# Performance work log

Measured on AMD Instinct MI355X. Metric: run time of the kernel, lower is better.

The kernel has to match this reference:

```python
import jax, jax.numpy as jnp
import numpy as np
import math

D_MODEL = 1024
N_HEADS = 16
D_HEAD = D_MODEL // N_HEADS
DECAY_MAX = 0.99  # buggy torch init: only the LAST head's decay rate survives the loop
LN_EPS = 1e-5


def setup_inputs() -> dict:
    key = jax.random.key(0)
    ks = jax.random.split(key, 12)
    B, S = 2, 2048
    x = jax.random.normal(ks[0], (B, S, D_MODEL), dtype=jnp.float32)
    def w(k):
        return jax.random.normal(k, (D_MODEL, D_MODEL), dtype=jnp.float32) * 0.02
    return {
        "x": x,
        "Wq": w(ks[1]), "bq": jnp.zeros((D_MODEL,), jnp.float32),
        "Wk": w(ks[2]), "bk": jnp.zeros((D_MODEL,), jnp.float32),
        "Wv": w(ks[3]), "bv": jnp.zeros((D_MODEL,), jnp.float32),
        "Wg": w(ks[4]), "bg": jnp.zeros((D_MODEL,), jnp.float32),
        "Wo": w(ks[5]), "bo": jnp.zeros((D_MODEL,), jnp.float32),
        "gamma": jnp.ones((D_MODEL,), jnp.float32),
        "beta": jnp.zeros((D_MODEL,), jnp.float32),
    }


def _decay_mask(S):
    # faithful to torch buffer: decay_matrix[i,j] = DECAY_MAX**(i-j) for j<=i else 0
    i = jnp.arange(S, dtype=jnp.float32)[:, None]
    j = jnp.arange(S, dtype=jnp.float32)[None, :]
    diff = i - j
    return jnp.where(diff >= 0, jnp.power(jnp.float32(DECAY_MAX), diff), 0.0)  # [S,S]


def reference(x, Wq, bq, Wk, bk, Wv, bv, Wg, bg, Wo, bo, gamma, beta):
    B, S, D = x.shape
    H, DH = N_HEADS, D_HEAD
    # projections -> [B,H,S,DH]
    Q = (x @ Wq + bq).reshape(B, S, H, DH).transpose(0, 2, 1, 3)
    K = (x @ Wk + bk).reshape(B, S, H, DH).transpose(0, 2, 1, 3)
    V = (x @ Wv + bv).reshape(B, S, H, DH).transpose(0, 2, 1, 3)
    scores = jnp.einsum('bhsd,bhtd->bhst', Q, K) / math.sqrt(DH)  # [B,H,S,S]
    mask = _decay_mask(S)  # [S,S], broadcast over B,H (head-independent per torch bug)
    retained = jnp.einsum('bhst,bhtd->bhsd', scores * mask, V)
    retained = retained.transpose(0, 2, 1, 3).reshape(B, S, D)
    # LayerNorm over last dim
    mu = jnp.mean(retained, axis=-1, keepdims=True)
    var = jnp.var(retained, axis=-1, keepdims=True)
    normed = (retained - mu) * jax.lax.rsqrt(var + LN_EPS) * gamma + beta
    G = jax.nn.sigmoid(x @ Wg + bg)
    return (normed * G) @ Wo + bo  # dropout = identity (eval)
```

## Files before the change

kernel.cpp:

```cpp
#include <hip/hip_runtime.h>

typedef __attribute__((ext_vector_type(4))) float f32x4;
typedef __attribute__((ext_vector_type(8))) short bf16x8;
typedef unsigned short USHORT;

static __device__ __forceinline__ float bf2f(USHORT u) {
    return __uint_as_float(((unsigned)u) << 16);
}
static __device__ __forceinline__ USHORT f2bf(float f) {
    unsigned u = __float_as_uint(f);
    unsigned r = u + 0x7FFF + ((u >> 16) & 1);
    return (USHORT)(r >> 16);
}

#define GLDS16(gp, lp) __builtin_amdgcn_global_load_lds(                      \
    (const __attribute__((address_space(1))) unsigned int*)(gp),              \
    (__attribute__((address_space(3))) unsigned int*)(lp), 16, 0, 0)

#define FULL_BARRIER() asm volatile("s_waitcnt vmcnt(0) lgkmcnt(0)\ns_barrier" ::: "memory")

#define D64 0.52559648f
#define L2D (-0.014499569695115089f)

struct PrepArgs { const float* src[5]; USHORT* dst[5]; const float* x; USHORT* xb; };

__global__ __launch_bounds__(256) void k_prep(PrepArgs pa) {
    const int z = blockIdx.z;
    const int tid = threadIdx.x;
    __shared__ USHORT t[64][65];
    if (z < 5) {
        const float* __restrict__ W  = pa.src[z];
        USHORT* __restrict__      WT = pa.dst[z];
        const int k0 = blockIdx.y * 64, n0 = blockIdx.x * 64;
#pragma unroll
        for (int s = 0; s < 4; s++) {
            int slot = tid + s * 256;
            int row = slot >> 4, c4 = (slot & 15) * 4;
            float4 vv = *(const float4*)&W[(size_t)(k0 + row) * 1024 + n0 + c4];
            t[row][c4 + 0] = f2bf(vv.x);
            t[row][c4 + 1] = f2bf(vv.y);
            t[row][c4 + 2] = f2bf(vv.z);
            t[row][c4 + 3] = f2bf(vv.w);
        }
        __syncthreads();
#pragma unroll
        for (int s = 0; s < 2; s++) {
            int slot = tid + s * 256;
            int n = slot >> 3, c8 = (slot & 7) * 8;
            USHORT tmp[8];
#pragma unroll
            for (int u = 0; u < 8; u++) tmp[u] = t[c8 + u][n];
            *(int4*)&WT[(size_t)(n0 + n) * 1024 + k0 + c8] = *(int4*)tmp;
        }
    } else {
        const int bi = blockIdx.y * 16 + blockIdx.x;
        const float* xs = pa.x + (size_t)bi * 16384;
        USHORT* xd = pa.xb + (size_t)bi * 16384;
#pragma unroll
        for (int u = 0; u < 16; u++) {
            int idx = u * 1024 + tid * 4;
            float4 v = *(const float4*)&xs[idx];
            *(ushort4*)&xd[idx] = make_ushort4(f2bf(v.x), f2bf(v.y), f2bf(v.z), f2bf(v.w));
        }
    }
}

struct GArgs {
    const USHORT* A;
    const USHORT* W[4];
    const float*  bias[4];
    void*         dst[4];
    USHORT*       dstv;
    float         scale[4];
    int           mode[4];
};


__global__ __launch_bounds__(256, 2) void k_gemm(GArgs ga) {
    const int z = blockIdx.z;
    const USHORT* __restrict__ A  = ga.A;
    const USHORT* __restrict__ BT = ga.W[z];
    __shared__ USHORT As[2][128 * 32];
    __shared__ USHORT Bs[2][128 * 32];
    const int tid = threadIdx.x;
    const int m0 = blockIdx.y * 128, n0 = blockIdx.x * 128;
    const int w = tid >> 6, l = tid & 63, lr = l & 15, q = l >> 4;
    const int wr = w >> 1, wc = w & 1;
    const int srow = tid >> 2, sco = (tid & 3) * 8;
    const int scol = (((tid & 3) ^ ((tid >> 3) & 3)) << 3);
    const int kread = ((q ^ ((lr >> 1) & 3)) << 3);
    f32x4 acc[4][4] = {};
    GLDS16(&A [(size_t)(m0 + srow)      * 1024 + scol], &As[0][srow * 32 + sco]);
    GLDS16(&A [(size_t)(m0 + srow + 64) * 1024 + scol], &As[0][(srow + 64) * 32 + sco]);
    GLDS16(&BT[(size_t)(n0 + srow)      * 1024 + scol], &Bs[0][srow * 32 + sco]);
    GLDS16(&BT[(size_t)(n0 + srow + 64) * 1024 + scol], &Bs[0][(srow + 64) * 32 + sco]);
    for (int kt = 0; kt < 32; kt++) {
        const int cur = kt & 1;
        FULL_BARRIER();
        if (kt + 1 < 32) {
            const int k1 = (kt + 1) * 32;
            const int nxt = 1 - cur;
            GLDS16(&A [(size_t)(m0 + srow)      * 1024 + k1 + scol], &As[nxt][srow * 32 + sco]);
            GLDS16(&A [(size_t)(m0 + srow + 64) * 1024 + k1 + scol], &As[nxt][(srow + 64) * 32 + sco]);
            GLDS16(&BT[(size_t)(n0 + srow)      * 1024 + k1 + scol], &Bs[nxt][srow * 32 + sco]);
            GLDS16(&BT[(size_t)(n0 + srow + 64) * 1024 + k1 + scol], &Bs[nxt][(srow + 64) * 32 + sco]);
        }
        bf16x8 af[4], bfr[4];
#pragma unroll
        for (int mi = 0; mi < 4; mi++)
            af[mi] = *(const bf16x8*)&As[cur][(wr * 64 + mi * 16 + lr) * 32 + kread];
#pragma unroll
        for (int ni = 0; ni < 4; ni++)
            bfr[ni] = *(const bf16x8*)&Bs[cur][(wc * 64 + ni * 16 + lr) * 32 + kread];
#pragma unroll
        for (int mi = 0; mi < 4; mi++)
#pragma unroll
            for (int ni = 0; ni < 4; ni++)
                acc[mi][ni] = __builtin_amdgcn_mfma_f32_16x16x32_bf16(
                    af[mi], bfr[ni], acc[mi][ni], 0, 0, 0);
    }
    const float scale = ga.scale[z];
    const int mode = ga.mode[z];
    const float* __restrict__ bias = ga.bias[z];
#pragma unroll
    for (int ni = 0; ni < 4; ni++) {
        int col = n0 + wc * 64 + ni * 16 + lr;
        float bv = bias[col];
#pragma unroll
        for (int mi = 0; mi < 4; mi++) {
            int r0 = m0 + wr * 64 + mi * 16 + q * 4;
            float vr[4];
#pragma unroll
            for (int r = 0; r < 4; r++) {
                float v = acc[mi][ni][r] + bv;
                if (mode == 1) v = 1.0f / (1.0f + __expf(-v));
                vr[r] = v * scale;
            }
            if (mode == 3) {
                float* df = (float*)ga.dst[z];
#pragma unroll
                for (int r = 0; r < 4; r++)
                    df[(size_t)(r0 + r) * 1024 + col] = vr[r];
            } else if (mode == 2) {
                int b = r0 >> 11, s = r0 & 2047;
                int h = col >> 6, d = col & 63;
                const float NP1 = 1.0101010101010102f;
                float c0 = exp2f(-L2D * (float)(s & 63));
                float c1 = c0 * NP1, c2 = c1 * NP1, c3 = c2 * NP1;
                *(ushort4*)&ga.dstv[(size_t)(((b * 16 + h) * 64) + d) * 2048 + s] =
                    make_ushort4(f2bf(vr[0] * c0), f2bf(vr[1] * c1),
                                 f2bf(vr[2] * c2), f2bf(vr[3] * c3));
            } else {
                USHORT* db = (USHORT*)ga.dst[z];
#pragma unroll
                for (int r = 0; r < 4; r++)
                    db[(size_t)(r0 + r) * 1024 + col] = f2bf(vr[r]);
            }
        }
    }
}

#define LDSA(buf, kh) (((buf) * 2 + (kh)) * 8192)
#define LDSB(buf, kh) (32768 + ((buf) * 2 + (kh)) * 8192)
#define BAR() asm volatile("s_barrier" ::: "memory")
#define VM8() asm volatile("s_waitcnt vmcnt(8)" ::: "memory")

#define STAGE_A(ks, kh, buf) do {                                             \
    const USHORT* s_ = aBase + (ks) * 64 + (kh) * 32;                         \
    GLDS16(s_,          &lds[LDSA(buf, kh) + ldsT]);                          \
    GLDS16(s_ + 131072, &lds[LDSA(buf, kh) + 4096 + ldsT]); } while (0)

#define STAGE_B(ks, kh, buf) do {                                             \
    const USHORT* s_ = bBase + (ks) * 64 + (kh) * 32;                         \
    GLDS16(s_,          &lds[LDSB(buf, kh) + ldsT]);                          \
    GLDS16(s_ + 131072, &lds[LDSB(buf, kh) + 4096 + ldsT]); } while (0)

#define PHASE256(buf, kh, mg, LOADB, STAGE_STMT, WAITSTMT) do {               \
    _Pragma("unroll")                                                         \
    for (int mi = 0; mi < 4; mi++)                                            \
        af[mi] = *(const bf16x8*)&lds[LDSA(buf, kh) + aoff + ((mg) * 4 + mi) * 512]; \
    if (LOADB) {                                                              \
        _Pragma("unroll")                                                     \
        for (int ni = 0; ni < 4; ni++)                                        \
            bfrag[ni] = *(const bf16x8*)&lds[LDSB(buf, kh) + boff + ni * 512];\
    }                                                                         \
    STAGE_STMT;                                                               \
    BAR();                                                                    \
    __builtin_amdgcn_s_setprio(1);                                            \
    _Pragma("unroll")                                                         \
    for (int mi = 0; mi < 4; mi++)                                            \
        _Pragma("unroll")                                                     \
        for (int ni = 0; ni < 4; ni++)                                        \
            acc[(mg) * 4 + mi][ni] = __builtin_amdgcn_mfma_f32_16x16x32_bf16( \
                af[mi], bfrag[ni], acc[(mg) * 4 + mi][ni], 0, 0, 0);          \
    __builtin_amdgcn_s_setprio(0);                                            \
    WAITSTMT;                                                                 \
    BAR();                                                                    \
} while (0)

__global__ __launch_bounds__(512, 2) void k_gemm256(GArgs ga) {
    extern __shared__ USHORT lds[];
    int bid = blockIdx.x + 4 * (blockIdx.y + 16 * blockIdx.z);
    bid = (bid & 7) * 32 + (bid >> 3);
    const int bz = bid >> 6;
    const int by = (bid >> 2) & 15;
    const int bx = bid & 3;
    const int z = bz;
    const USHORT* __restrict__ A  = ga.A;
    const USHORT* __restrict__ BT = ga.W[z];
    const int m0 = by * 256, n0 = bx * 256;
    const int tid = threadIdx.x;
    const int wid = tid >> 6, l = tid & 63, lr = l & 15, q = l >> 4;
    const int wr = wid >> 2, wc = wid & 3;
    const int srow = tid >> 2;
    const int scol = (((tid & 3) ^ ((tid >> 3) & 3)) << 3);
    const USHORT* aBase = A  + (size_t)(m0 + srow) * 1024 + scol;
    const USHORT* bBase = BT + (size_t)(n0 + srow) * 1024 + scol;
    const int ldsT = tid * 8;
    const int kread = ((q ^ ((lr >> 1) & 3)) << 3);
    const int aoff = (wr * 128 + lr) * 32 + kread;
    const int boff = (wc * 64 + lr) * 32 + kread;
    f32x4 acc[8][4] = {};
    bf16x8 af[4], bfrag[4];

    STAGE_A(0, 0, 0); STAGE_B(0, 0, 0);
    STAGE_A(0, 1, 0); STAGE_B(0, 1, 0);
    STAGE_A(1, 0, 1); STAGE_B(1, 0, 1);
    VM8();
    BAR();

    for (int kt = 0; kt < 16; kt += 2) {
        const int ks1 = kt + 1;
        const int ks2 = (kt + 2 < 16) ? kt + 2 : 15;
        const int ks3 = (kt + 2 < 16) ? kt + 2 : 15;
        const int ks4 = (kt + 3 < 16) ? kt + 3 : 15;
        PHASE256(0, 0, 0, 1, STAGE_A(ks1, 1, 1), (void)0);
        PHASE256(0, 0, 1, 0, STAGE_B(ks1, 1, 1), VM8());
        PHASE256(0, 1, 0, 1, STAGE_A(ks2, 0, 0), (void)0);
        PHASE256(0, 1, 1, 0, STAGE_B(ks2, 0, 0), VM8());
        PHASE256(1, 0, 0, 1, STAGE_A(ks3, 1, 0), (void)0);
        PHASE256(1, 0, 1, 0, STAGE_B(ks3, 1, 0), VM8());
        PHASE256(1, 1, 0, 1, STAGE_A(ks4, 0, 1), (void)0);
        PHASE256(1, 1, 1, 0, STAGE_B(ks4, 0, 1), VM8());
    }

    const float scale = ga.scale[z];
    const int mode = ga.mode[z];
    const float* __restrict__ bias = ga.bias[z];
#pragma unroll
    for (int ni = 0; ni < 4; ni++) {
        int col = n0 + wc * 64 + ni * 16 + lr;
        float bv = bias[col];
#pragma unroll
        for (int mi = 0; mi < 8; mi++) {
            int r0 = m0 + wr * 128 + mi * 16 + q * 4;
            float vr[4];
#pragma unroll
            for (int r = 0; r < 4; r++) {
                float v = acc[mi][ni][r] + bv;
                if (mode == 1) v = 1.0f / (1.0f + __expf(-v));
                vr[r] = v * scale;
            }
            if (mode == 3) {
                float* df = (float*)ga.dst[z];
#pragma unroll
                for (int r = 0; r < 4; r++)
                    df[(size_t)(r0 + r) * 1024 + col] = vr[r];
            } else if (mode == 2) {
                int b = r0 >> 11, s = r0 & 2047;
                int h = col >> 6, d = col & 63;
                const float NP1 = 1.0101010101010102f;
                float c0 = exp2f(-L2D * (float)(s & 63));
                float c1 = c0 * NP1, c2 = c1 * NP1, c3 = c2 * NP1;
                *(ushort4*)&ga.dstv[(size_t)(((b * 16 + h) * 64) + d) * 2048 + s] =
                    make_ushort4(f2bf(vr[0] * c0), f2bf(vr[1] * c1),
                                 f2bf(vr[2] * c2), f2bf(vr[3] * c3));
            } else {
                USHORT* db = (USHORT*)ga.dst[z];
#pragma unroll
                for (int r = 0; r < 4; r++)
                    db[(size_t)(r0 + r) * 1024 + col] = f2bf(vr[r]);
            }
        }
    }
}

__global__ __launch_bounds__(256) void k_attn_u(const USHORT* __restrict__ K,
                                                const USHORT* __restrict__ VT,
                                                float* __restrict__ U) {
    const int bh = blockIdx.x, c = blockIdx.y;
    const int b = bh >> 4, h = bh & 15;
    const int tid = threadIdx.x, w = tid >> 6, l = tid & 63, lr = l & 15, q = l >> 4;
    __shared__ USHORT KT[64 * 72];
    __shared__ USHORT Vs[64 * 72];
#pragma unroll
    for (int s = 0; s < 2; s++) {
        int slot = tid + s * 256;
        int row = slot >> 3, co = (slot & 7) * 8;
        USHORT kv[8];
        *(int4*)kv = *(const int4*)&K[(size_t)(b * 2048 + c * 64 + row) * 1024 + h * 64 + co];
#pragma unroll
        for (int u = 0; u < 8; u++) KT[(co + u) * 72 + row] = kv[u];
        *(int4*)&Vs[row * 72 + co] =
            *(const int4*)&VT[(size_t)(bh * 64 + row) * 2048 + c * 64 + co];
    }
    __syncthreads();
    f32x4 acc[4] = {};
    bf16x8 av[2];
#pragma unroll
    for (int kk = 0; kk < 2; kk++)
        av[kk] = *(const bf16x8*)&Vs[(w * 16 + lr) * 72 + kk * 32 + q * 8];
#pragma unroll
    for (int dkt = 0; dkt < 4; dkt++)
#pragma unroll
        for (int kk = 0; kk < 2; kk++) {
            bf16x8 bk = *(const bf16x8*)&KT[(dkt * 16 + lr) * 72 + kk * 32 + q * 8];
            acc[dkt] = __builtin_amdgcn_mfma_f32_16x16x32_bf16(av[kk], bk, acc[dkt], 0, 0, 0);
        }
    float* slot = U + (size_t)(bh * 32 + c) * 4096;
#pragma unroll
    for (int dkt = 0; dkt < 4; dkt++)
#pragma unroll
        for (int r = 0; r < 4; r++)
            slot[(w * 16 + q * 4 + r) * 64 + dkt * 16 + lr] = acc[dkt][r] * D64;
}

__global__ __launch_bounds__(256) void k_scan(float* __restrict__ U) {
    const int bh = blockIdx.x;
    const int idx4 = blockIdx.y * 256 + threadIdx.x;
    float* base = U + (size_t)bh * 32 * 4096 + idx4 * 4;
    float4 s = make_float4(0.f, 0.f, 0.f, 0.f);
    for (int c = 0; c < 32; c++) {
        float* p = base + (size_t)c * 4096;
        float4 v = *(const float4*)p;
        s.x = s.x * D64 + v.x;
        s.y = s.y * D64 + v.y;
        s.z = s.z * D64 + v.z;
        s.w = s.w * D64 + v.w;
        *(float4*)p = s;
    }
}

__global__ __launch_bounds__(256, 2) void k_apply(const USHORT* __restrict__ Q,
                                                  const USHORT* __restrict__ K,
                                                  const USHORT* __restrict__ VT,
                                                  const float* __restrict__ U,
                                                  USHORT* __restrict__ R,
                                                  float* __restrict__ stats) {
    const int bh = blockIdx.x, c = blockIdx.y;
    const int b = bh >> 4, h = bh & 15;
    const int i0 = c * 64;
    const int tid = threadIdx.x, w = tid >> 6, l = tid & 63, lr = l & 15, q = l >> 4;
    __shared__ USHORT Qs[64 * 72];
    __shared__ USHORT Ks[64 * 72];
    __shared__ USHORT Vs[64 * 72];
    __shared__ USHORT Ps[4][16 * 72];
    __shared__ unsigned Spk[4096];
#pragma unroll
    for (int s = 0; s < 2; s++) {
        int slot = tid + s * 256;
        int row = slot >> 3, c8 = (slot & 7) * 8;
        USHORT q8[8];
        *(int4*)q8 = *(const int4*)&Q[(size_t)(b * 2048 + i0 + row) * 1024 + h * 64 + c8];
        const float fr = exp2f(L2D * (float)row);
#pragma unroll
        for (int u = 0; u < 8; u++) q8[u] = f2bf(bf2f(q8[u]) * fr);
        *(int4*)&Qs[row * 72 + c8] = *(int4*)q8;
        *(int4*)&Ks[row * 72 + c8] =
            *(const int4*)&K[(size_t)(b * 2048 + i0 + row) * 1024 + h * 64 + c8];
        *(int4*)&Vs[row * 72 + c8] =
            *(const int4*)&VT[(size_t)(bh * 64 + row) * 2048 + i0 + c8];
    }
    if (c > 0) {
        const float* p = U + (size_t)(bh * 32 + (c - 1)) * 4096 + tid * 16;
        float sa[16];
#pragma unroll
        for (int u4 = 0; u4 < 4; u4++) {
            float4 uv = *(const float4*)(p + u4 * 4);
            sa[u4 * 4 + 0] = uv.x; sa[u4 * 4 + 1] = uv.y;
            sa[u4 * 4 + 2] = uv.z; sa[u4 * 4 + 3] = uv.w;
        }
#pragma unroll
        for (int u = 0; u < 16; u++) {
            USHORT hi = f2bf(sa[u]);
            float  lo = sa[u] - bf2f(hi);
            Spk[tid * 16 + u] = (unsigned)hi | ((unsigned)f2bf(lo) << 16);
        }
    }
    __syncthreads();
    bf16x8 bqf[2];
#pragma unroll
    for (int kk = 0; kk < 2; kk++)
        bqf[kk] = *(const bf16x8*)&Qs[(w * 16 + lr) * 72 + kk * 32 + q * 8];
    f32x4 accr[4] = {};
    if (c > 0) {
#pragma unroll
        for (int dt = 0; dt < 4; dt++)
#pragma unroll
            for (int kk = 0; kk < 2; kk++) {
                const unsigned* sp = &Spk[(dt * 16 + lr) * 64 + kk * 32 + q * 8];
                uint4 pa = *(const uint4*)sp;
                uint4 pb = *(const uint4*)(sp + 4);
                unsigned pk[8] = { pa.x, pa.y, pa.z, pa.w, pb.x, pb.y, pb.z, pb.w };
                bf16x8 hi, lo;
#pragma unroll
                for (int u = 0; u < 8; u++) {
                    hi[u] = (short)(pk[u] & 0xffffu);
                    lo[u] = (short)(pk[u] >> 16);
                }
                accr[dt] = __builtin_amdgcn_mfma_f32_16x16x32_bf16(hi, bqf[kk], accr[dt], 0, 0, 0);
                accr[dt] = __builtin_amdgcn_mfma_f32_16x16x32_bf16(lo, bqf[kk], accr[dt], 0, 0, 0);
            }
    }
    {
        f32x4 accp[4] = {};
#pragma unroll
        for (int kk = 0; kk < 2; kk++)
#pragma unroll
            for (int jt = 0; jt < 4; jt++) {
                bf16x8 akf = *(const bf16x8*)&Ks[(jt * 16 + lr) * 72 + kk * 32 + q * 8];
                accp[jt] = __builtin_amdgcn_mfma_f32_16x16x32_bf16(akf, bqf[kk], accp[jt], 0, 0, 0);
            }
        const int ii = w * 16 + lr;
#pragma unroll
        for (int jt = 0; jt < 4; jt++) {
            const int jj = jt * 16 + q * 4;
            float v0 = (jj + 0 <= ii) ? accp[jt][0] : 0.0f;
            float v1 = (jj + 1 <= ii) ? accp[jt][1] : 0.0f;
            float v2 = (jj + 2 <= ii) ? accp[jt][2] : 0.0f;
            float v3 = (jj + 3 <= ii) ? accp[jt][3] : 0.0f;
            unsigned w0 = __builtin_amdgcn_perm(
                __float_as_uint(v1), __float_as_uint(v0), 0x07060302u);
            unsigned w1 = __builtin_amdgcn_perm(
                __float_as_uint(v3), __float_as_uint(v2), 0x07060302u);
            *(uint2*)&Ps[w][lr * 72 + jt * 16 + q * 4] = make_uint2(w0, w1);
        }
        asm volatile("s_waitcnt lgkmcnt(0)" ::: "memory");
#pragma unroll
        for (int kk = 0; kk < 2; kk++) {
            bf16x8 bpf = *(const bf16x8*)&Ps[w][lr * 72 + kk * 32 + q * 8];
#pragma unroll
            for (int dt = 0; dt < 4; dt++) {
                bf16x8 avf = *(const bf16x8*)&Vs[(dt * 16 + lr) * 72 + kk * 32 + q * 8];
                accr[dt] = __builtin_amdgcn_mfma_f32_16x16x32_bf16(avf, bpf, accr[dt], 0, 0, 0);
            }
        }
    }
    {
        float s1 = 0.f, s2 = 0.f;
#pragma unroll
        for (int dt = 0; dt < 4; dt++)
#pragma unroll
            for (int r = 0; r < 4; r++) {
                float v = accr[dt][r];
                s1 += v; s2 += v * v;
            }
        s1 += __shfl_down(s1, 32); s2 += __shfl_down(s2, 32);
        s1 += __shfl_down(s1, 16); s2 += __shfl_down(s2, 16);
        if (q == 0) {
            int row = b * 2048 + i0 + w * 16 + lr;
            *(float2*)&stats[((size_t)row * 16 + h) * 2] = make_float2(s1, s2);
        }
    }
    {
        const int i = i0 + w * 16 + lr;
#pragma unroll
        for (int dt = 0; dt < 4; dt++) {
            f32x4 a = accr[dt];
            *(ushort4*)&R[(size_t)(b * 2048 + i) * 1024 + h * 64 + dt * 16 + q * 4] =
                make_ushort4(f2bf(a[0]), f2bf(a[1]), f2bf(a[2]), f2bf(a[3]));
        }
    }
}

__global__ __launch_bounds__(256) void k_ln_gate(const USHORT* __restrict__ R,
                                                 const USHORT* __restrict__ G,
                                                 const float* __restrict__ stats,
                                                 const float* __restrict__ gamma,
                                                 const float* __restrict__ beta,
                                                 USHORT* __restrict__ NG) {
    const int row = blockIdx.x, tid = threadIdx.x;
    float s1 = 0.f, s2 = 0.f;
    const float* sp = &stats[(size_t)row * 32];
#pragma unroll
    for (int hh = 0; hh < 8; hh++) {
        float4 v = *(const float4*)(sp + hh * 4);
        s1 += v.x + v.z; s2 += v.y + v.w;
    }
    const float mu  = s1 * (1.0f / 1024.0f);
    const float var = s2 * (1.0f / 1024.0f) - mu * mu;
    const float inv = rsqrtf(fmaxf(var, 0.0f) + 1e-5f);
    ushort4 rv = *(const ushort4*)&R[(size_t)row * 1024 + tid * 4];
    ushort4 g4 = *(const ushort4*)&G[(size_t)row * 1024 + tid * 4];
    float4 gm = *(const float4*)&gamma[tid * 4];
    float4 bt = *(const float4*)&beta[tid * 4];
    float  vv[4]  = { bf2f(rv.x), bf2f(rv.y), bf2f(rv.z), bf2f(rv.w) };
    USHORT gg[4]  = { g4.x, g4.y, g4.z, g4.w };
    float  gmm[4] = { gm.x, gm.y, gm.z, gm.w };
    float  btt[4] = { bt.x, bt.y, bt.z, bt.w };
    USHORT o4[4];
#pragma unroll
    for (int u = 0; u < 4; u++) {
        float nv = (vv[u] - mu) * inv * gmm[u] + btt[u];
        o4[u] = f2bf(nv * bf2f(gg[u]));
    }
    *(ushort4*)&NG[(size_t)row * 1024 + tid * 4] = make_ushort4(o4[0], o4[1], o4[2], o4[3]);
}

extern "C" void kernel_launch(void* const* d_in, const int* in_sizes, int n_in,
                              void* d_out, int out_size, void* d_ws, size_t ws_size,
                              hipStream_t stream) {
    const float* x     = (const float*)d_in[0];
    const float* Wq    = (const float*)d_in[1];
    const float* bq    = (const float*)d_in[2];
    const float* Wk    = (const float*)d_in[3];
    const float* bk    = (const float*)d_in[4];
    const float* Wv    = (const float*)d_in[5];
    const float* bv    = (const float*)d_in[6];
    const float* Wg    = (const float*)d_in[7];
    const float* bg    = (const float*)d_in[8];
    const float* Wo    = (const float*)d_in[9];
    const float* bo    = (const float*)d_in[10];
    const float* gamma = (const float*)d_in[11];
    const float* beta  = (const float*)d_in[12];

    char* ws = (char*)d_ws;
    const size_t MB = 1 << 20;
    USHORT* WqT = (USHORT*)(ws + 0 * MB);
    USHORT* WkT = (USHORT*)(ws + 2 * MB);
    USHORT* WvT = (USHORT*)(ws + 4 * MB);
    USHORT* WgT = (USHORT*)(ws + 6 * MB);
    USHORT* WoT = (USHORT*)(ws + 8 * MB);
    USHORT* Qb  = (USHORT*)(ws + 10 * MB);
    USHORT* Kb  = (USHORT*)(ws + 18 * MB);
    USHORT* VTb = (USHORT*)(ws + 26 * MB);
    USHORT* Gb  = (USHORT*)(ws + 34 * MB);
    float*  Sts = (float*) (ws + 42 * MB);
    USHORT* NGb = Qb;
    USHORT* Xb  = (USHORT*)d_out;
    float*  Ust = (float*)d_out;

    {
        PrepArgs pa;
        pa.src[0] = Wq; pa.src[1] = Wk; pa.src[2] = Wv; pa.src[3] = Wg; pa.src[4] = Wo;
        pa.dst[0] = WqT; pa.dst[1] = WkT; pa.dst[2] = WvT; pa.dst[3] = WgT; pa.dst[4] = WoT;
        pa.x = x; pa.xb = Xb;
        k_prep<<<dim3(16, 16, 6), 256, 0, stream>>>(pa);
    }
    {
        static int s_256ok = -1;
        if (s_256ok < 0) {
            hipError_t e = hipFuncSetAttribute(
                reinterpret_cast<const void*>(&k_gemm256),
                hipFuncAttributeMaxDynamicSharedMemorySize, 131072);
            s_256ok = (e == hipSuccess) ? 1 : 0;
        }
        GArgs ga;
        ga.A = Xb;
        ga.W[0] = WqT; ga.W[1] = WkT; ga.W[2] = WvT; ga.W[3] = WgT;
        ga.bias[0] = bq; ga.bias[1] = bk; ga.bias[2] = bv; ga.bias[3] = bg;
        ga.dst[0] = Qb; ga.dst[1] = Kb; ga.dst[2] = nullptr; ga.dst[3] = Gb;
        ga.dstv = VTb;
        ga.scale[0] = 0.125f; ga.scale[1] = 1.0f; ga.scale[2] = 1.0f; ga.scale[3] = 1.0f;
        ga.mode[0] = 0; ga.mode[1] = 0; ga.mode[2] = 2; ga.mode[3] = 1;
        if (s_256ok)
            k_gemm256<<<dim3(4, 16, 4), 512, 131072, stream>>>(ga);
        else
            k_gemm<<<dim3(8, 32, 4), 256, 0, stream>>>(ga);
    }
    k_attn_u<<<dim3(32, 32), 256, 0, stream>>>(Kb, VTb, Ust);
    k_scan<<<dim3(32, 4), 256, 0, stream>>>(Ust);
    k_apply<<<dim3(32, 32), 256, 0, stream>>>(Qb, Kb, VTb, Ust, Kb, Sts);
    k_ln_gate<<<4096, 256, 0, stream>>>(Kb, Gb, Sts, gamma, beta, NGb);
    {
        GArgs go;
        go.A = NGb;
        for (int i = 0; i < 4; i++) {
            go.W[i] = WoT; go.bias[i] = bo; go.dst[i] = d_out;
            go.scale[i] = 1.0f; go.mode[i] = 3;
        }
        go.dstv = nullptr;
        k_gemm<<<dim3(8, 32, 1), 256, 0, stream>>>(go);
    }
}
```

Baseline: 214.4 us.

## Fold Q decay into GEMM epilogue, pack scan state, use direct-to-LDS swizzled loads

The per-row decay factor on Q moves out of k_apply into the projection GEMM epilogue through a new mode 4. k_scan now writes its state as packed bf16 hi/lo pairs, so k_apply no longer converts it. k_attn_u and k_apply load tiles straight into LDS with global_load_lds using XOR-swizzled unpadded layouts, in place of register staging with padded rows. This cuts VALU conversion work and register round-trips in the attention kernels. The cost is extra epilogue math in the GEMM and a state buffer whose meaning is now reinterpreted between kernels.

```diff
diff --git a/kernel.cpp b/kernel.cpp
--- a/kernel.cpp
+++ b/kernel.cpp
@@ -74,7 +74,6 @@
     float         scale[4];
     int           mode[4];
 };
-
 
 __global__ __launch_bounds__(256, 2) void k_gemm(GArgs ga) {
     const int z = blockIdx.z;
@@ -130,11 +129,14 @@
         for (int mi = 0; mi < 4; mi++) {
             int r0 = m0 + wr * 64 + mi * 16 + q * 4;
             float vr[4];
+            float d0 = (mode == 4) ? exp2f(L2D * (float)(r0 & 63)) : 1.0f;
 #pragma unroll
             for (int r = 0; r < 4; r++) {
                 float v = acc[mi][ni][r] + bv;
                 if (mode == 1) v = 1.0f / (1.0f + __expf(-v));
-                vr[r] = v * scale;
+                v *= scale;
+                if (mode == 4) { v *= d0; d0 *= 0.99f; }
+                vr[r] = v;
             }
             if (mode == 3) {
                 float* df = (float*)ga.dst[z];
@@ -255,11 +257,14 @@
         for (int mi = 0; mi < 8; mi++) {
             int r0 = m0 + wr * 128 + mi * 16 + q * 4;
             float vr[4];
+            float d0 = (mode == 4) ? exp2f(L2D * (float)(r0 & 63)) : 1.0f;
 #pragma unroll
             for (int r = 0; r < 4; r++) {
                 float v = acc[mi][ni][r] + bv;
                 if (mode == 1) v = 1.0f / (1.0f + __expf(-v));
-                vr[r] = v * scale;
+                v *= scale;
+                if (mode == 4) { v *= d0; d0 *= 0.99f; }
+                vr[r] = v;
             }
             if (mode == 3) {
                 float* df = (float*)ga.dst[z];
@@ -292,7 +297,7 @@
     const int b = bh >> 4, h = bh & 15;
     const int tid = threadIdx.x, w = tid >> 6, l = tid & 63, lr = l & 15, q = l >> 4;
     __shared__ USHORT KT[64 * 72];
-    __shared__ USHORT Vs[64 * 72];
+    __shared__ USHORT Vs[64 * 64];
 #pragma unroll
     for (int s = 0; s < 2; s++) {
         int slot = tid + s * 256;
@@ -300,23 +305,32 @@
         USHORT kv[8];
         *(int4*)kv = *(const int4*)&K[(size_t)(b * 2048 + c * 64 + row) * 1024 + h * 64 + co];
 #pragma unroll
-        for (int u = 0; u < 8; u++) KT[(co + u) * 72 + row] = kv[u];
-        *(int4*)&Vs[row * 72 + co] =
-            *(const int4*)&VT[(size_t)(bh * 64 + row) * 2048 + c * 64 + co];
-    }
-    __syncthreads();
+        for (int u = 0; u < 8; u++) {
+            int d = co + u;
+            KT[d * 72 + ((((row >> 3) ^ ((d >> 3) & 7)) << 3) | (row & 7))] = kv[u];
+        }
+        int r_ = slot >> 3, j_ = slot & 7;
+        int js_ = ((j_ ^ (r_ & 7)) << 3);
+        GLDS16(&VT[(size_t)(bh * 64 + r_) * 2048 + c * 64 + js_], &Vs[slot * 8]);
+    }
+    FULL_BARRIER();
     f32x4 acc[4] = {};
     bf16x8 av[2];
-#pragma unroll
-    for (int kk = 0; kk < 2; kk++)
-        av[kk] = *(const bf16x8*)&Vs[(w * 16 + lr) * 72 + kk * 32 + q * 8];
-#pragma unroll
-    for (int dkt = 0; dkt < 4; dkt++)
+    {
+        const int row = w * 16 + lr;
+#pragma unroll
+        for (int kk = 0; kk < 2; kk++)
+            av[kk] = *(const bf16x8*)&Vs[row * 64 + (((kk * 4 + q) ^ (row & 7)) << 3)];
+    }
+#pragma unroll
+    for (int dkt = 0; dkt < 4; dkt++) {
+        const int dp = dkt * 16 + lr;
 #pragma unroll
         for (int kk = 0; kk < 2; kk++) {
-            bf16x8 bk = *(const bf16x8*)&KT[(dkt * 16 + lr) * 72 + kk * 32 + q * 8];
+            bf16x8 bk = *(const bf16x8*)&KT[dp * 72 + (((kk * 4 + q) ^ ((dp >> 3) & 7)) << 3)];
             acc[dkt] = __builtin_amdgcn_mfma_f32_16x16x32_bf16(av[kk], bk, acc[dkt], 0, 0, 0);
         }
+    }
     float* slot = U + (size_t)(bh * 32 + c) * 4096;
 #pragma unroll
     for (int dkt = 0; dkt < 4; dkt++)
@@ -337,68 +351,69 @@
         s.y = s.y * D64 + v.y;
         s.z = s.z * D64 + v.z;
         s.w = s.w * D64 + v.w;
-        *(float4*)p = s;
+        unsigned pk[4];
+        const float sv[4] = { s.x, s.y, s.z, s.w };
+#pragma unroll
+        for (int u = 0; u < 4; u++) {
+            USHORT hi = f2bf(sv[u]);
+            float  lo = sv[u] - bf2f(hi);
+            pk[u] = (unsigned)hi | ((unsigned)f2bf(lo) << 16);
+        }
+        *(uint4*)p = make_uint4(pk[0], pk[1], pk[2], pk[3]);
     }
 }
 
 __global__ __launch_bounds__(256, 2) void k_apply(const USHORT* __restrict__ Q,
                                                   const USHORT* __restrict__ K,
                                                   const USHORT* __restrict__ VT,
-                                                  const float* __restrict__ U,
+                                                  const unsigned* __restrict__ Sp,
                                                   USHORT* __restrict__ R,
                                                   float* __restrict__ stats) {
     const int bh = blockIdx.x, c = blockIdx.y;
     const int b = bh >> 4, h = bh & 15;
     const int i0 = c * 64;
     const int tid = threadIdx.x, w = tid >> 6, l = tid & 63, lr = l & 15, q = l >> 4;
-    __shared__ USHORT Qs[64 * 72];
-    __shared__ USHORT Ks[64 * 72];
-    __shared__ USHORT Vs[64 * 72];
+    __shared__ USHORT Qs[64 * 64];
+    __shared__ USHORT Ks[64 * 64];
+    __shared__ USHORT Vs[64 * 64];
     __shared__ USHORT Ps[4][16 * 72];
     __shared__ unsigned Spk[4096];
 #pragma unroll
     for (int s = 0; s < 2; s++) {
-        int slot = tid + s * 256;
-        int row = slot >> 3, c8 = (slot & 7) * 8;
-        USHORT q8[8];
-        *(int4*)q8 = *(const int4*)&Q[(size_t)(b * 2048 + i0 + row) * 1024 + h * 64 + c8];
-        const float fr = exp2f(L2D * (float)row);
-#pragma unroll
-        for (int u = 0; u < 8; u++) q8[u] = f2bf(bf2f(q8[u]) * fr);
-        *(int4*)&Qs[row * 72 + c8] = *(int4*)q8;
-        *(int4*)&Ks[row * 72 + c8] =
-            *(const int4*)&K[(size_t)(b * 2048 + i0 + row) * 1024 + h * 64 + c8];
-        *(int4*)&Vs[row * 72 + c8] =
-            *(const int4*)&VT[(size_t)(bh * 64 + row) * 2048 + i0 + c8];
+        int C = tid + s * 256;
+        int r_ = C >> 3, j_ = C & 7;
+        int js_ = ((j_ ^ (r_ & 7)) << 3);
+        GLDS16(&Q [(size_t)(b * 2048 + i0 + r_) * 1024 + h * 64 + js_], &Qs[C * 8]);
+        GLDS16(&K [(size_t)(b * 2048 + i0 + r_) * 1024 + h * 64 + js_], &Ks[C * 8]);
+        GLDS16(&VT[(size_t)(bh * 64 + r_) * 2048 + i0 + js_],           &Vs[C * 8]);
     }
     if (c > 0) {
-        const float* p = U + (size_t)(bh * 32 + (c - 1)) * 4096 + tid * 16;
-        float sa[16];
-#pragma unroll
-        for (int u4 = 0; u4 < 4; u4++) {
-            float4 uv = *(const float4*)(p + u4 * 4);
-            sa[u4 * 4 + 0] = uv.x; sa[u4 * 4 + 1] = uv.y;
-            sa[u4 * 4 + 2] = uv.z; sa[u4 * 4 + 3] = uv.w;
-        }
-#pragma unroll
-        for (int u = 0; u < 16; u++) {
-            USHORT hi = f2bf(sa[u]);
-            float  lo = sa[u] - bf2f(hi);
-            Spk[tid * 16 + u] = (unsigned)hi | ((unsigned)f2bf(lo) << 16);
-        }
-    }
-    __syncthreads();
+        const unsigned* sb = Sp + (size_t)(bh * 32 + (c - 1)) * 4096;
+#pragma unroll
+        for (int s = 0; s < 4; s++) {
+            int C = tid + s * 256;
+            int r_ = C >> 4, j_ = C & 15;
+            int js_ = ((j_ ^ ((r_ & 7) << 1)) << 2);
+            GLDS16(&sb[r_ * 64 + js_], &Spk[C * 4]);
+        }
+    }
+    FULL_BARRIER();
     bf16x8 bqf[2];
-#pragma unroll
-    for (int kk = 0; kk < 2; kk++)
-        bqf[kk] = *(const bf16x8*)&Qs[(w * 16 + lr) * 72 + kk * 32 + q * 8];
+    {
+        const int row = w * 16 + lr;
+#pragma unroll
+        for (int kk = 0; kk < 2; kk++)
+            bqf[kk] = *(const bf16x8*)&Qs[row * 64 + (((kk * 4 + q) ^ (row & 7)) << 3)];
+    }
     f32x4 accr[4] = {};
     if (c > 0) {
 #pragma unroll
-        for (int dt = 0; dt < 4; dt++)
+        for (int dt = 0; dt < 4; dt++) {
+            const int row = dt * 16 + lr;
 #pragma unroll
             for (int kk = 0; kk < 2; kk++) {
-                const unsigned* sp = &Spk[(dt * 16 + lr) * 64 + kk * 32 + q * 8];
+                const unsigned* sp =
+                    &Spk[row * 64 + ((((kk << 3) + (q << 1)) ^ ((row & 7) << 1)) << 2)];
                 uint4 pa = *(const uint4*)sp;
                 uint4 pb = *(const uint4*)(sp + 4);
                 unsigned pk[8] = { pa.x, pa.y, pa.z, pa.w, pb.x, pb.y, pb.z, pb.w };
@@ -411,6 +426,7 @@
                 accr[dt] = __builtin_amdgcn_mfma_f32_16x16x32_bf16(hi, bqf[kk], accr[dt], 0, 0, 0);
                 accr[dt] = __builtin_amdgcn_mfma_f32_16x16x32_bf16(lo, bqf[kk], accr[dt], 0, 0, 0);
             }
+        }
     }
     {
         f32x4 accp[4] = {};
@@ -418,7 +434,8 @@
         for (int kk = 0; kk < 2; kk++)
 #pragma unroll
             for (int jt = 0; jt < 4; jt++) {
-                bf16x8 akf = *(const bf16x8*)&Ks[(jt * 16 + lr) * 72 + kk * 32 + q * 8];
+                const int row = jt * 16 + lr;
+                bf16x8 akf = *(const bf16x8*)&Ks[row * 64 + (((kk * 4 + q) ^ (row & 7)) << 3)];
                 accp[jt] = __builtin_amdgcn_mfma_f32_16x16x32_bf16(akf, bqf[kk], accp[jt], 0, 0, 0);
             }
         const int ii = w * 16 + lr;
@@ -441,7 +458,8 @@
             bf16x8 bpf = *(const bf16x8*)&Ps[w][lr * 72 + kk * 32 + q * 8];
 #pragma unroll
             for (int dt = 0; dt < 4; dt++) {
-                bf16x8 avf = *(const bf16x8*)&Vs[(dt * 16 + lr) * 72 + kk * 32 + q * 8];
+                const int row = dt * 16 + lr;
+                bf16x8 avf = *(const bf16x8*)&Vs[row * 64 + (((kk * 4 + q) ^ (row & 7)) << 3)];
                 accr[dt] = __builtin_amdgcn_mfma_f32_16x16x32_bf16(avf, bpf, accr[dt], 0, 0, 0);
             }
         }
@@ -562,7 +580,7 @@
         ga.dst[0] = Qb; ga.dst[1] = Kb; ga.dst[2] = nullptr; ga.dst[3] = Gb;
         ga.dstv = VTb;
         ga.scale[0] = 0.125f; ga.scale[1] = 1.0f; ga.scale[2] = 1.0f; ga.scale[3] = 1.0f;
-        ga.mode[0] = 0; ga.mode[1] = 0; ga.mode[2] = 2; ga.mode[3] = 1;
+        ga.mode[0] = 4; ga.mode[1] = 0; ga.mode[2] = 2; ga.mode[3] = 1;
         if (s_256ok)
             k_gemm256<<<dim3(4, 16, 4), 512, 131072, stream>>>(ga);
         else
@@ -570,7 +588,7 @@
     }
     k_attn_u<<<dim3(32, 32), 256, 0, stream>>>(Kb, VTb, Ust);
     k_scan<<<dim3(32, 4), 256, 0, stream>>>(Ust);
-    k_apply<<<dim3(32, 32), 256, 0, stream>>>(Qb, Kb, VTb, Ust, Kb, Sts);
+    k_apply<<<dim3(32, 32), 256, 0, stream>>>(Qb, Kb, VTb, (const unsigned*)Ust, Kb, Sts);
     k_ln_gate<<<4096, 256, 0, stream>>>(Kb, Gb, Sts, gamma, beta, NGb);
     {
         GArgs go;
```

New measurement: 221.6 us. 1.03x slower.
